# Optimization experiments

Hardware: AMD Instinct MI355X
Metric: run time of the kernel (lower is better)

Reference implementation:

```python
import jax, jax.numpy as jnp
import numpy as np

FP16_MAX = 65504.0  # clamp_fp16 bound
GROUP = 64          # SVDQuant int4 group size along in_features


def _int4_quant_dequant(w):
    """Symmetric per-(out_channel, group) int4 fake-quant of a weight [out, in].
    Emulates the W4 weight numerics of SVDQW4A4Linear at the dequantized level."""
    o, i = w.shape
    wg = w.reshape(o, i // GROUP, GROUP)
    scale = np.max(np.abs(wg), axis=-1, keepdims=True) / 7.0
    scale = np.where(scale == 0.0, 1.0, scale)
    q = np.clip(np.round(wg / scale), -8, 7)
    return (q * scale).reshape(o, i).astype(np.float32)


def setup_inputs() -> dict:
    dim, hidden = 3072, 8192
    B, S = 2, 4096
    rng = np.random.default_rng(0)
    # fused [w1; w3] weight: [2*hidden, dim]; down proj w2: [dim, hidden]
    w13 = _int4_quant_dequant((rng.standard_normal((2 * hidden, dim)) * 0.02).astype(np.float32))
    w2 = _int4_quant_dequant((rng.standard_normal((dim, hidden)) * 0.02).astype(np.float32))
    key = jax.random.key(0)
    x = jax.random.normal(key, (B, S, dim), dtype=jnp.float32)
    return {"x": x, "w13": jnp.asarray(w13), "w2": jnp.asarray(w2)}


def reference(x, w13, w2):
    # fused gate/up projection: [B,S,dim] @ [2H,dim]^T -> [B,S,2H]
    h = jnp.einsum("bsd,hd->bsh", x, w13)
    # NOTE: original code does `x3, x1 = x.chunk(2, dim=-1)` -> first half is x3
    x3, x1 = jnp.split(h, 2, axis=-1)
    g = jnp.clip(jax.nn.silu(x1) * x3, -FP16_MAX, FP16_MAX)  # clamp_fp16
    # down projection: [B,S,H] @ [dim,H]^T -> [B,S,dim]
    return jnp.einsum("bsh,dh->bsd", g, w2)
```

## Files before the change

### kernel.cpp

```cpp
#include <hip/hip_runtime.h>
#include <hip/hip_bf16.h>


typedef __attribute__((ext_vector_type(8))) __bf16 bf16x8;
typedef __attribute__((ext_vector_type(4))) float f32x4;

#define GLD_LDS16(gptr, lptr)                                                        \
  __builtin_amdgcn_global_load_lds(                                                  \
      (const __attribute__((address_space(1))) void*)(gptr),                         \
      (__attribute__((address_space(3))) void*)(lptr), 16, 0, 0)

#define VMCNT(n) asm volatile("s_waitcnt vmcnt(" #n ")" ::: "memory")
#define BAR()    __builtin_amdgcn_s_barrier()

#define MFMA16(a, b, c) __builtin_amdgcn_mfma_f32_16x16x32_bf16((a), (b), (c), 0, 0, 0)

__device__ __forceinline__ __bf16 bfr(float f) {
  unsigned int u = __builtin_bit_cast(unsigned int, f);
  unsigned short r = (unsigned short)((u + 0x7FFFu + ((u >> 16) & 1u)) >> 16);
  return __builtin_bit_cast(__bf16, r);
}

__global__ __launch_bounds__(256)
void k_cvt(const float* __restrict__ src, unsigned short* __restrict__ dst, long n) {
  long i = ((long)blockIdx.x * 256 + threadIdx.x) * 8;
  const long stride = (long)gridDim.x * 256 * 8;
  for (; i < n; i += stride) {
    float4 f0 = *(const float4*)(src + i);
    float4 f1 = *(const float4*)(src + i + 4);
    bf16x8 o;
    o[0] = bfr(f0.x); o[1] = bfr(f0.y); o[2] = bfr(f0.z); o[3] = bfr(f0.w);
    o[4] = bfr(f1.x); o[5] = bfr(f1.y); o[6] = bfr(f1.z); o[7] = bfr(f1.w);
    *(bf16x8*)(dst + i) = o;
  }
}

__global__ __launch_bounds__(512, 2)
void k_gateup13(const unsigned short* __restrict__ X,
                const unsigned short* __restrict__ W13,
                __hip_bfloat16* __restrict__ G)
{
  constexpr int K = 3072, LDG = 8192, NT = K / 64;
  __shared__ unsigned short lds[65536];

  const int t = threadIdx.x, l = t & 63, wid = t >> 6;
  const int wm = wid >> 2, wn = wid & 3;
  const int l15 = l & 15, lhi = l >> 4, sw = l15 & 7;

  const int bid = blockIdx.x;
  const int swz = (bid & 7) * 256 + (bid >> 3);
  const int mb = swz >> 6, nb = swz & 63;

  const int srow = t >> 3;
  const int scol = ((t & 7) ^ (srow & 7)) * 8;
  const unsigned short* xa = X   + (size_t)(mb * 256 + srow) * K + scol;
  const unsigned short* b3 = W13 + (size_t)(nb * 128 + srow) * K + scol;
  const unsigned short* b1 = W13 + (size_t)(8192 + nb * 128 + srow) * K + scol;
  const int lo = t * 8;

#define STG_A(d, kt) do {                                                      \
    GLD_LDS16(xa + (kt),                  lds + (d) * 32768 + lo);             \
    GLD_LDS16(xa + (size_t)64 * K + (kt),  lds + (d) * 32768 + 4096 + lo);     \
    GLD_LDS16(xa + (size_t)128 * K + (kt), lds + (d) * 32768 + 8192 + lo);     \
    GLD_LDS16(xa + (size_t)192 * K + (kt), lds + (d) * 32768 + 12288 + lo);    \
  } while (0)
#define STG_B3(d, kt) do {                                                     \
    GLD_LDS16(b3 + (kt),                 lds + (d) * 32768 + 16384 + lo);      \
    GLD_LDS16(b3 + (size_t)64 * K + (kt), lds + (d) * 32768 + 20480 + lo);     \
  } while (0)
#define STG_B1(d, kt) do {                                                     \
    GLD_LDS16(b1 + (kt),                 lds + (d) * 32768 + 24576 + lo);      \
    GLD_LDS16(b1 + (size_t)64 * K + (kt), lds + (d) * 32768 + 28672 + lo);     \
  } while (0)

  f32x4 acc3[8][2], acc1[8][2];
#pragma unroll
  for (int m = 0; m < 8; ++m)
#pragma unroll
    for (int n = 0; n < 2; ++n) {
      acc3[m][n] = (f32x4){0.f, 0.f, 0.f, 0.f};
      acc1[m][n] = (f32x4){0.f, 0.f, 0.f, 0.f};
    }

  STG_A(0, 0); STG_B3(0, 0); STG_B1(0, 0);

  for (int c = 0; c < NT; ++c) {
    const int R = c & 1, S = R ^ 1;
    const int kn = (c + 1 < NT ? c + 1 : 0) * 64;
    const int Ab = R * 32768, B3b = Ab + 16384, B1b = Ab + 24576;

    VMCNT(2);
    BAR();
    bf16x8 ra[8][2], r3[2][2];
#pragma unroll
    for (int mf = 0; mf < 8; ++mf)
#pragma unroll
      for (int kk = 0; kk < 2; ++kk) {
        const int row = wm * 128 + mf * 16 + l15;
        ra[mf][kk] = *(const bf16x8*)(lds + Ab + row * 64 + ((kk * 4 + lhi) ^ sw) * 8);
      }
#pragma unroll
    for (int nf = 0; nf < 2; ++nf)
#pragma unroll
      for (int kk = 0; kk < 2; ++kk) {
        const int row = wn * 32 + nf * 16 + l15;
        r3[nf][kk] = *(const bf16x8*)(lds + B3b + row * 64 + ((kk * 4 + lhi) ^ sw) * 8);
      }
    STG_A(S, kn); STG_B3(S, kn);
    __builtin_amdgcn_s_setprio(1);
#pragma unroll
    for (int mf = 0; mf < 8; ++mf)
#pragma unroll
      for (int nf = 0; nf < 2; ++nf)
#pragma unroll
        for (int kk = 0; kk < 2; ++kk)
          acc3[mf][nf] = MFMA16(ra[mf][kk], r3[nf][kk], acc3[mf][nf]);
    __builtin_amdgcn_s_setprio(0);

    VMCNT(6);
    BAR();
    bf16x8 r1[2][2];
#pragma unroll
    for (int nf = 0; nf < 2; ++nf)
#pragma unroll
      for (int kk = 0; kk < 2; ++kk) {
        const int row = wn * 32 + nf * 16 + l15;
        r1[nf][kk] = *(const bf16x8*)(lds + B1b + row * 64 + ((kk * 4 + lhi) ^ sw) * 8);
      }
    STG_B1(S, kn);
    __builtin_amdgcn_s_setprio(1);
#pragma unroll
    for (int mf = 0; mf < 8; ++mf)
#pragma unroll
      for (int nf = 0; nf < 2; ++nf)
#pragma unroll
        for (int kk = 0; kk < 2; ++kk)
          acc1[mf][nf] = MFMA16(ra[mf][kk], r1[nf][kk], acc1[mf][nf]);
    __builtin_amdgcn_s_setprio(0);
  }

  const int gr0 = mb * 256 + wm * 128;
  const int gc0 = nb * 128 + wn * 32;
#pragma unroll
  for (int mf = 0; mf < 8; ++mf)
#pragma unroll
    for (int nf = 0; nf < 2; ++nf)
#pragma unroll
      for (int r = 0; r < 4; ++r) {
        float h3 = acc3[mf][nf][r];
        float h1 = acc1[mf][nf][r];
        float s  = h1 / (1.f + __expf(-h1));
        float g  = fminf(fmaxf(s * h3, -65504.f), 65504.f);
        G[(size_t)(gr0 + mf * 16 + lhi * 4 + r) * LDG + (gc0 + nf * 16 + l15)] =
            __float2bfloat16(g);
      }
#undef STG_A
#undef STG_B3
#undef STG_B1
}

__global__ __launch_bounds__(512, 2)
void k_down11(const unsigned short* __restrict__ Gm,
              const unsigned short* __restrict__ W2,
              float* __restrict__ Out)
{
  constexpr int K = 8192, LDO = 3072, NT = K / 64;
  __shared__ unsigned short lds[73728];

  const int t = threadIdx.x, l = t & 63, wid = t >> 6;
  const int wm = wid >> 1, wn = wid & 1;
  const int l15 = l & 15, lhi = l >> 4, sw = l15 & 7;

  const int bid = blockIdx.x;
  const int swz = (bid & 7) * 96 + (bid >> 3);
  const int mb = swz / 24, nb = swz % 24;

  const int srow = t >> 3;
  const int scol = ((t & 7) ^ (srow & 7)) * 8;
  const unsigned short* ga = Gm + (size_t)(mb * 256 + srow) * K + scol;
  const unsigned short* wb = W2 + (size_t)(nb * 128 + srow) * K + scol;
  const int lo = t * 8;

#define DST_A(e, kt) do {                                                       \
    GLD_LDS16(ga + (kt),                 lds + (e) * 16384 + lo);               \
    GLD_LDS16(ga + (size_t)64 * K + (kt),  lds + (e) * 16384 + 4096 + lo);      \
    GLD_LDS16(ga + (size_t)128 * K + (kt), lds + (e) * 16384 + 8192 + lo);      \
    GLD_LDS16(ga + (size_t)192 * K + (kt), lds + (e) * 16384 + 12288 + lo);     \
  } while (0)
#define DST_B(e, kt) do {                                                       \
    GLD_LDS16(wb + (kt),                lds + 49152 + (e) * 8192 + lo);         \
    GLD_LDS16(wb + (size_t)64 * K + (kt), lds + 49152 + (e) * 8192 + 4096 + lo); \
  } while (0)

  f32x4 acc[4][4];
#pragma unroll
  for (int mf = 0; mf < 4; ++mf)
#pragma unroll
    for (int nf = 0; nf < 4; ++nf)
      acc[mf][nf] = (f32x4){0.f, 0.f, 0.f, 0.f};

  DST_B(0, 0);  DST_A(0, 0);
  DST_B(1, 64); DST_A(1, 64);

  for (int c = 0; c < NT; ++c) {
    const int e = c % 3;
    const int eS = (c + 2) % 3;
    const int k2 = (c + 2 < NT ? c + 2 : 0) * 64;

    VMCNT(6);
    BAR();

    bf16x8 ra[4][2], rb[4][2];
#pragma unroll
    for (int mf = 0; mf < 4; ++mf)
#pragma unroll
      for (int kk = 0; kk < 2; ++kk)
        ra[mf][kk] = *(const bf16x8*)(lds + e * 16384 + (wm * 64 + mf * 16 + l15) * 64 + ((kk * 4 + lhi) ^ sw) * 8);
#pragma unroll
    for (int nf = 0; nf < 4; ++nf)
#pragma unroll
      for (int kk = 0; kk < 2; ++kk)
        rb[nf][kk] = *(const bf16x8*)(lds + 49152 + e * 8192 + (wn * 64 + nf * 16 + l15) * 64 + ((kk * 4 + lhi) ^ sw) * 8);

    DST_B(eS, k2);
    DST_A(eS, k2);

    __builtin_amdgcn_s_setprio(1);
#pragma unroll
    for (int mf = 0; mf < 4; ++mf)
#pragma unroll
      for (int nf = 0; nf < 4; ++nf)
#pragma unroll
        for (int kk = 0; kk < 2; ++kk)
          acc[mf][nf] = MFMA16(ra[mf][kk], rb[nf][kk], acc[mf][nf]);
    __builtin_amdgcn_s_setprio(0);
  }

  const int r0 = mb * 256 + wm * 64;
  const int c0 = nb * 128 + wn * 64;
#pragma unroll
  for (int mf = 0; mf < 4; ++mf)
#pragma unroll
    for (int nf = 0; nf < 4; ++nf)
#pragma unroll
      for (int r = 0; r < 4; ++r)
        Out[(size_t)(r0 + mf * 16 + lhi * 4 + r) * LDO + (c0 + nf * 16 + l15)] =
            acc[mf][nf][r];
#undef DST_A
#undef DST_B
}

extern "C" void kernel_launch(void* const* d_in, const int* in_sizes, int n_in,
                              void* d_out, int out_size, void* d_ws, size_t ws_size,
                              hipStream_t stream) {
  const float* x   = (const float*)d_in[0];
  const float* w13 = (const float*)d_in[1];
  const float* w2  = (const float*)d_in[2];
  float* out = (float*)d_out;

  const long NX = 25165824L, NW13 = 50331648L, NW2 = 25165824L;
  const size_t XB = 50331648, W13B = 100663296, W2B = 50331648;

  unsigned short* xb   = (unsigned short*)d_ws;
  unsigned short* w13b = (unsigned short*)((char*)d_ws + XB);
  unsigned short* w2b  = (unsigned short*)((char*)d_ws + XB + W13B);
  __hip_bfloat16* g    = (__hip_bfloat16*)((char*)d_ws + XB + W13B + W2B);

  k_cvt<<<2048, 256, 0, stream>>>(x,   xb,   NX);
  k_cvt<<<2048, 256, 0, stream>>>(w13, w13b, NW13);
  k_cvt<<<2048, 256, 0, stream>>>(w2,  w2b,  NW2);
  k_gateup13<<<2048, 512, 0, stream>>>(xb, w13b, g);
  k_down11<<<768, 512, 0, stream>>>((const unsigned short*)g, w2b, out);
}
```

Measured before the change: 1.145 ms.

## Halve gate/up M tile and switch to triple-buffered LDS pipeline

The gate/up kernel's M tile drops from 256 to 128 rows, so the grid doubles to 4096 blocks. Its K loop moves from a two-phase double buffer to a three-stage ring buffer that prefetches two k-steps ahead. There is now one barrier per iteration, and the gate and up MFMAs are interleaved. The aim is to hide global-load latency and cut barrier stalls, but each block does less arithmetic per byte loaded, so arithmetic intensity falls and the X and W13 tiles must be loaded more often.

```diff
diff --git a/kernel.cpp b/kernel.cpp
--- a/kernel.cpp
+++ b/kernel.cpp
@@ -36,67 +36,68 @@
 }
 
 __global__ __launch_bounds__(512, 2)
-void k_gateup13(const unsigned short* __restrict__ X,
+void k_gateup14(const unsigned short* __restrict__ X,
                 const unsigned short* __restrict__ W13,
                 __hip_bfloat16* __restrict__ G)
 {
   constexpr int K = 3072, LDG = 8192, NT = K / 64;
-  __shared__ unsigned short lds[65536];
+  __shared__ unsigned short lds[73728];
 
   const int t = threadIdx.x, l = t & 63, wid = t >> 6;
   const int wm = wid >> 2, wn = wid & 3;
   const int l15 = l & 15, lhi = l >> 4, sw = l15 & 7;
 
   const int bid = blockIdx.x;
-  const int swz = (bid & 7) * 256 + (bid >> 3);
+  const int swz = (bid & 7) * 512 + (bid >> 3);
   const int mb = swz >> 6, nb = swz & 63;
 
   const int srow = t >> 3;
   const int scol = ((t & 7) ^ (srow & 7)) * 8;
-  const unsigned short* xa = X   + (size_t)(mb * 256 + srow) * K + scol;
+  const unsigned short* xa = X   + (size_t)(mb * 128 + srow) * K + scol;
   const unsigned short* b3 = W13 + (size_t)(nb * 128 + srow) * K + scol;
   const unsigned short* b1 = W13 + (size_t)(8192 + nb * 128 + srow) * K + scol;
   const int lo = t * 8;
 
-#define STG_A(d, kt) do {                                                      \
-    GLD_LDS16(xa + (kt),                  lds + (d) * 32768 + lo);             \
-    GLD_LDS16(xa + (size_t)64 * K + (kt),  lds + (d) * 32768 + 4096 + lo);     \
-    GLD_LDS16(xa + (size_t)128 * K + (kt), lds + (d) * 32768 + 8192 + lo);     \
-    GLD_LDS16(xa + (size_t)192 * K + (kt), lds + (d) * 32768 + 12288 + lo);    \
-  } while (0)
-#define STG_B3(d, kt) do {                                                     \
-    GLD_LDS16(b3 + (kt),                 lds + (d) * 32768 + 16384 + lo);      \
-    GLD_LDS16(b3 + (size_t)64 * K + (kt), lds + (d) * 32768 + 20480 + lo);     \
-  } while (0)
-#define STG_B1(d, kt) do {                                                     \
-    GLD_LDS16(b1 + (kt),                 lds + (d) * 32768 + 24576 + lo);      \
-    GLD_LDS16(b1 + (size_t)64 * K + (kt), lds + (d) * 32768 + 28672 + lo);     \
-  } while (0)
-
-  f32x4 acc3[8][2], acc1[8][2];
-#pragma unroll
-  for (int m = 0; m < 8; ++m)
+#define GST_A(e, kt) do {                                                       \
+    GLD_LDS16(xa + (kt),                  lds + (e) * 24576 + lo);              \
+    GLD_LDS16(xa + (size_t)64 * K + (kt),  lds + (e) * 24576 + 4096 + lo);      \
+  } while (0)
+#define GST_B3(e, kt) do {                                                      \
+    GLD_LDS16(b3 + (kt),                  lds + (e) * 24576 + 8192 + lo);       \
+    GLD_LDS16(b3 + (size_t)64 * K + (kt),  lds + (e) * 24576 + 12288 + lo);     \
+  } while (0)
+#define GST_B1(e, kt) do {                                                      \
+    GLD_LDS16(b1 + (kt),                  lds + (e) * 24576 + 16384 + lo);      \
+    GLD_LDS16(b1 + (size_t)64 * K + (kt),  lds + (e) * 24576 + 20480 + lo);     \
+  } while (0)
+
+  f32x4 acc3[4][2], acc1[4][2];
+#pragma unroll
+  for (int m = 0; m < 4; ++m)
 #pragma unroll
     for (int n = 0; n < 2; ++n) {
       acc3[m][n] = (f32x4){0.f, 0.f, 0.f, 0.f};
       acc1[m][n] = (f32x4){0.f, 0.f, 0.f, 0.f};
     }
 
-  STG_A(0, 0); STG_B3(0, 0); STG_B1(0, 0);
+  GST_A(0, 0);  GST_B3(0, 0);  GST_B1(0, 0);
+  GST_A(1, 64); GST_B3(1, 64); GST_B1(1, 64);
 
   for (int c = 0; c < NT; ++c) {
-    const int R = c & 1, S = R ^ 1;
-    const int kn = (c + 1 < NT ? c + 1 : 0) * 64;
-    const int Ab = R * 32768, B3b = Ab + 16384, B1b = Ab + 24576;
-
-    VMCNT(2);
+    const int e = c % 3;
+    const int eS = (c + 2) % 3;
+    const int k2 = (c + 2 < NT ? c + 2 : 0) * 64;
+    const int Ab = e * 24576, B3b = Ab + 8192, B1b = Ab + 16384;
+
+    VMCNT(6);
     BAR();
-    bf16x8 ra[8][2], r3[2][2];
-#pragma unroll
-    for (int mf = 0; mf < 8; ++mf)
+
+    bf16x8 ra[4][2], r3[2][2], r1[2][2];
+#pragma unroll
+    for (int mf = 0; mf < 4; ++mf)
 #pragma unroll
       for (int kk = 0; kk < 2; ++kk) {
-        const int row = wm * 128 + mf * 16 + l15;
+        const int row = wm * 64 + mf * 16 + l15;
         ra[mf][kk] = *(const bf16x8*)(lds + Ab + row * 64 + ((kk * 4 + lhi) ^ sw) * 8);
       }
 #pragma unroll
@@ -105,44 +106,28 @@
       for (int kk = 0; kk < 2; ++kk) {
         const int row = wn * 32 + nf * 16 + l15;
         r3[nf][kk] = *(const bf16x8*)(lds + B3b + row * 64 + ((kk * 4 + lhi) ^ sw) * 8);
-      }
-    STG_A(S, kn); STG_B3(S, kn);
-    __builtin_amdgcn_s_setprio(1);
-#pragma unroll
-    for (int mf = 0; mf < 8; ++mf)
-#pragma unroll
-      for (int nf = 0; nf < 2; ++nf)
-#pragma unroll
-        for (int kk = 0; kk < 2; ++kk)
-          acc3[mf][nf] = MFMA16(ra[mf][kk], r3[nf][kk], acc3[mf][nf]);
-    __builtin_amdgcn_s_setprio(0);
-
-    VMCNT(6);
-    BAR();
-    bf16x8 r1[2][2];
-#pragma unroll
-    for (int nf = 0; nf < 2; ++nf)
-#pragma unroll
-      for (int kk = 0; kk < 2; ++kk) {
-        const int row = wn * 32 + nf * 16 + l15;
         r1[nf][kk] = *(const bf16x8*)(lds + B1b + row * 64 + ((kk * 4 + lhi) ^ sw) * 8);
       }
-    STG_B1(S, kn);
+
+    GST_A(eS, k2); GST_B3(eS, k2); GST_B1(eS, k2);
+
     __builtin_amdgcn_s_setprio(1);
 #pragma unroll
-    for (int mf = 0; mf < 8; ++mf)
+    for (int mf = 0; mf < 4; ++mf)
 #pragma unroll
       for (int nf = 0; nf < 2; ++nf)
 #pragma unroll
-        for (int kk = 0; kk < 2; ++kk)
+        for (int kk = 0; kk < 2; ++kk) {
+          acc3[mf][nf] = MFMA16(ra[mf][kk], r3[nf][kk], acc3[mf][nf]);
           acc1[mf][nf] = MFMA16(ra[mf][kk], r1[nf][kk], acc1[mf][nf]);
+        }
     __builtin_amdgcn_s_setprio(0);
   }
 
-  const int gr0 = mb * 256 + wm * 128;
+  const int gr0 = mb * 128 + wm * 64;
   const int gc0 = nb * 128 + wn * 32;
 #pragma unroll
-  for (int mf = 0; mf < 8; ++mf)
+  for (int mf = 0; mf < 4; ++mf)
 #pragma unroll
     for (int nf = 0; nf < 2; ++nf)
 #pragma unroll
@@ -154,9 +139,9 @@
         G[(size_t)(gr0 + mf * 16 + lhi * 4 + r) * LDG + (gc0 + nf * 16 + l15)] =
             __float2bfloat16(g);
       }
-#undef STG_A
-#undef STG_B3
-#undef STG_B1
+#undef GST_A
+#undef GST_B3
+#undef GST_B1
 }
 
 __global__ __launch_bounds__(512, 2)
@@ -269,6 +254,6 @@
   k_cvt<<<2048, 256, 0, stream>>>(x,   xb,   NX);
   k_cvt<<<2048, 256, 0, stream>>>(w13, w13b, NW13);
   k_cvt<<<2048, 256, 0, stream>>>(w2,  w2b,  NW2);
-  k_gateup13<<<2048, 512, 0, stream>>>(xb, w13b, g);
+  k_gateup14<<<4096, 512, 0, stream>>>(xb, w13b, g);
   k_down11<<<768, 512, 0, stream>>>((const unsigned short*)g, w2b, out);
 }
```

Result: slower. 1.397 ms (+22.0%).
